# Optimization experiments

Measured on AMD Instinct MI355X. Metric: run time of the kernel, lower is better.

The kernel has to match this reference:

```python
import jax, jax.numpy as jnp
import numpy as np

N_NODES = 100000
IN_DIM = 128
HIDDEN = 256
N_CLASSES = 16
N_EDGES = 1600000
N_GRAPHS = 64


def setup_inputs() -> dict:
    key = jax.random.key(0)
    ks = jax.random.split(key, 12)
    x = jax.random.normal(ks[0], (N_NODES, IN_DIM), dtype=jnp.float32)
    edge_index = jax.random.randint(ks[1], (2, N_EDGES), 0, N_NODES, dtype=jnp.int64)
    batch = jnp.sort(jax.random.randint(ks[2], (N_NODES,), 0, N_GRAPHS, dtype=jnp.int64))
    s = 0.05
    # SAGEConv layer 1: lin_l (on aggregated neighbors, with bias), lin_r (on root, no bias)
    W1l = jax.random.normal(ks[3], (IN_DIM, HIDDEN), dtype=jnp.float32) * s
    b1 = jnp.zeros((HIDDEN,), dtype=jnp.float32)
    W1r = jax.random.normal(ks[4], (IN_DIM, HIDDEN), dtype=jnp.float32) * s
    # SAGEConv layer 2
    W2l = jax.random.normal(ks[5], (HIDDEN, HIDDEN), dtype=jnp.float32) * s
    b2 = jnp.zeros((HIDDEN,), dtype=jnp.float32)
    W2r = jax.random.normal(ks[6], (HIDDEN, HIDDEN), dtype=jnp.float32) * s
    # final classifier
    fcW = jax.random.normal(ks[7], (HIDDEN, N_CLASSES), dtype=jnp.float32) * s
    fcb = jnp.zeros((N_CLASSES,), dtype=jnp.float32)
    return {"x": x, "edge_index": edge_index, "batch": batch,
            "W1l": W1l, "b1": b1, "W1r": W1r,
            "W2l": W2l, "b2": b2, "W2r": W2r,
            "fcW": fcW, "fcb": fcb}


def _sage_conv(x, src, dst, Wl, bl, Wr, n_nodes):
    # mean aggregation of neighbor features onto destination nodes
    agg = jax.ops.segment_sum(x[src], dst, num_segments=n_nodes)      # [N, d]
    deg = jax.ops.segment_sum(jnp.ones(src.shape, x.dtype), dst, num_segments=n_nodes)
    mean = agg / jnp.maximum(deg, 1.0)[:, None]
    # out = lin_l(mean_neighbors) + lin_r(x_root)  (PyG SAGEConv, mean aggr)
    return mean @ Wl + bl + x @ Wr


def reference(x, edge_index, batch, W1l, b1, W1r, W2l, b2, W2r, fcW, fcb):
    src, dst = edge_index[0], edge_index[1]
    h = jax.nn.relu(_sage_conv(x, src, dst, W1l, b1, W1r, N_NODES))
    # dropout is identity in inference mode
    h = jax.nn.relu(_sage_conv(h, src, dst, W2l, b2, W2r, N_NODES))
    # global mean pool over graphs in the batch
    g_sum = jax.ops.segment_sum(h, batch, num_segments=N_GRAPHS)      # [G, d]
    g_cnt = jax.ops.segment_sum(jnp.ones(batch.shape, h.dtype), batch, num_segments=N_GRAPHS)
    g = g_sum / jnp.maximum(g_cnt, 1.0)[:, None]
    return g @ fcW + fcb                                              # [G, num_classes]
```

## Files before the change

kernel.cpp:

```cpp
#include <hip/hip_runtime.h>

#define INDIM 128
#define HID 256
#define NCLS 16
#define NGRAPH 64
#define CHUNK 8192

typedef __bf16 bf16_t;
typedef bf16_t bf16x8 __attribute__((ext_vector_type(8)));
typedef float f32x4 __attribute__((ext_vector_type(4)));

__device__ __forceinline__ float bfu_lo(unsigned v) {
    union { unsigned i; float f; } u; u.i = v << 16; return u.f;
}
__device__ __forceinline__ float bfu_hi(unsigned v) {
    union { unsigned i; float f; } u; u.i = v & 0xffff0000u; return u.f;
}
__device__ __forceinline__ unsigned short f2bf(float f) {
    union { float f; unsigned i; } u; u.f = f;
    unsigned b = u.i;
    return (unsigned short)((b + 0x7fffu + ((b >> 16) & 1u)) >> 16);
}
__device__ __forceinline__ unsigned packbf(float lo, float hi) {
    return (unsigned)f2bf(lo) | ((unsigned)f2bf(hi) << 16);
}

typedef __attribute__((address_space(1))) const unsigned gu32_t;
typedef __attribute__((address_space(3))) unsigned lu32_t;
__device__ __forceinline__ void gl_lds16(const void* g, void* l) {
    __builtin_amdgcn_global_load_lds((gu32_t*)g, (lu32_t*)l, 16, 0, 0);
}

#define IACC(aE, aO, v)                              \
    do {                                             \
        aE[0] += ((v).x & 0x00FF00FFu);              \
        aO[0] += (((v).x >> 8) & 0x00FF00FFu);       \
        aE[1] += ((v).y & 0x00FF00FFu);              \
        aO[1] += (((v).y >> 8) & 0x00FF00FFu);       \
        aE[2] += ((v).z & 0x00FF00FFu);              \
        aO[2] += (((v).z >> 8) & 0x00FF00FFu);       \
        aE[3] += ((v).w & 0x00FF00FFu);              \
        aO[3] += (((v).w >> 8) & 0x00FF00FFu);       \
    } while (0)

__global__ void hist_kernel(const int* __restrict__ dst, int* __restrict__ deg, int E) {
    int e = blockIdx.x * blockDim.x + threadIdx.x;
    if (e < E) atomicAdd(&deg[dst[e]], 1);
}

__global__ void scan1_kernel(const int* __restrict__ deg, int* __restrict__ bsum, int n) {
    __shared__ int s[256];
    int t = threadIdx.x;
    int i = blockIdx.x * 256 + t;
    s[t] = (i < n) ? deg[i] : 0;
    __syncthreads();
    for (int off = 128; off > 0; off >>= 1) {
        if (t < off) s[t] += s[t + off];
        __syncthreads();
    }
    if (t == 0) bsum[blockIdx.x] = s[0];
}

__global__ void scan2_kernel(int* bsum, int nb) {
    __shared__ int s[1024];
    int t = threadIdx.x;
    int v = (t < nb) ? bsum[t] : 0;
    s[t] = v;
    __syncthreads();
    for (int off = 1; off < 1024; off <<= 1) {
        int u = (t >= off) ? s[t - off] : 0;
        __syncthreads();
        s[t] += u;
        __syncthreads();
    }
    if (t < nb) bsum[t] = s[t] - v;
}

__global__ void scan3_kernel(const int* __restrict__ deg, const int* __restrict__ bsum,
                             int* __restrict__ offs, int* __restrict__ gcur, int n) {
    __shared__ int s[256];
    int t = threadIdx.x;
    int i = blockIdx.x * 256 + t;
    int v = (i < n) ? deg[i] : 0;
    s[t] = v;
    __syncthreads();
    for (int off = 1; off < 256; off <<= 1) {
        int u = (t >= off) ? s[t - off] : 0;
        __syncthreads();
        s[t] += u;
        __syncthreads();
    }
    if (i < n) offs[i] = s[t] - v + bsum[blockIdx.x];
    if (t == 0) gcur[blockIdx.x] = bsum[blockIdx.x];
}

__global__ __launch_bounds__(256) void binA_kernel(const int* __restrict__ src,
                                                   const int* __restrict__ dst,
                                                   int* __restrict__ gcur,
                                                   unsigned* __restrict__ tmp,
                                                   int E, int nbuck) {
    __shared__ int hist[512];
    __shared__ int base[512];
    int t = threadIdx.x;
    int e0 = blockIdx.x * CHUNK;
    int e1 = min(e0 + CHUNK, E);
    for (int i = t; i < nbuck; i += 256) hist[i] = 0;
    __syncthreads();
    for (int e = e0 + t; e < e1; e += 256) atomicAdd(&hist[dst[e] >> 8], 1);
    __syncthreads();
    for (int i = t; i < nbuck; i += 256) {
        int c = hist[i];
        base[i] = (c > 0) ? atomicAdd(&gcur[i], c) : 0;
    }
    __syncthreads();
    for (int e = e0 + t; e < e1; e += 256) {
        int d = dst[e];
        int p = atomicAdd(&base[d >> 8], 1);
        tmp[p] = ((unsigned)(d & 255) << 17) | (unsigned)src[e];
    }
}

__global__ __launch_bounds__(256) void binB_kernel(const unsigned* __restrict__ tmp,
                                                   const int* __restrict__ offs,
                                                   int* __restrict__ srclist, int E, int n) {
    __shared__ int cur[256];
    int b = blockIdx.x;
    int node0 = b << 8;
    int nnodes = min(256, n - node0);
    int t = threadIdx.x;
    if (t < nnodes) cur[t] = offs[node0 + t];
    __syncthreads();
    int ebeg = offs[node0];
    int eend = (node0 + 256 < n) ? offs[node0 + 256] : E;
    for (int e = ebeg + t; e < eend; e += 256) {
        unsigned v = tmp[e];
        int p = atomicAdd(&cur[v >> 17], 1);
        srclist[p] = (int)(v & 0x1FFFFu);
    }
}

__global__ void prep_kernel(const float* __restrict__ x, unsigned short* __restrict__ xb,
                            const float* __restrict__ W1l, const float* __restrict__ W1r,
                            unsigned short* __restrict__ Bt1,
                            const float* __restrict__ W2l, const float* __restrict__ W2r,
                            unsigned short* __restrict__ Bt2, float* __restrict__ pmaxx,
                            int castb) {
    __shared__ float wmax[4];
    int b = blockIdx.x, t = threadIdx.x;
    if (b < castb) {
        int i4 = (b * 256 + t) * 4;
        float4 v = *(const float4*)(x + i4);
        *(ushort4*)(xb + i4) = make_ushort4(f2bf(v.x), f2bf(v.y), f2bf(v.z), f2bf(v.w));
        float m = fmaxf(fmaxf(fabsf(v.x), fabsf(v.y)), fmaxf(fabsf(v.z), fabsf(v.w)));
#pragma unroll
        for (int off = 32; off > 0; off >>= 1) m = fmaxf(m, __shfl_xor(m, off));
        if ((t & 63) == 0) wmax[t >> 6] = m;
        __syncthreads();
        if (t == 0)
            pmaxx[b] = fmaxf(fmaxf(wmax[0], wmax[1]), fmaxf(wmax[2], wmax[3]));
    } else if (b < castb + 256) {
        int idx = (b - castb) * 256 + t;
        int nn = idx >> 8, k = idx & 255;
        float v = (k < 128) ? W1l[(size_t)k * 256 + nn] : W1r[(size_t)(k - 128) * 256 + nn];
        Bt1[(size_t)nn * 256 + k] = f2bf(v);
    } else {
        int idx = (b - castb - 256) * 256 + t;
        int nn = idx >> 9, k = idx & 511;
        float v = (k < 256) ? W2l[(size_t)k * 256 + nn] : W2r[(size_t)(k - 256) * 256 + nn];
        Bt2[(size_t)nn * 512 + k] = f2bf(v);
    }
}

__global__ void reducemax_kernel(const float* __restrict__ pmax, int cnt,
                                 float* __restrict__ gmax) {
    __shared__ float wmax[4];
    int t = threadIdx.x;
    float m = 0.f;
    for (int i = t; i < cnt; i += 256) m = fmaxf(m, pmax[i]);
#pragma unroll
    for (int off = 32; off > 0; off >>= 1) m = fmaxf(m, __shfl_xor(m, off));
    if ((t & 63) == 0) wmax[t >> 6] = m;
    __syncthreads();
    if (t == 0) gmax[0] = fmaxf(fmaxf(wmax[0], wmax[1]), fmaxf(wmax[2], wmax[3]));
}

__global__ void quantx_kernel(const float* __restrict__ x, const float* __restrict__ gmaxp,
                              unsigned* __restrict__ xq, int total4) {
    int idx = blockIdx.x * blockDim.x + threadIdx.x;
    if (idx >= total4) return;
    float inv = 127.f / fmaxf(*gmaxp, 1e-20f);
    float4 v = *(const float4*)(x + idx * 4);
    int b0 = (int)fminf(fmaxf(rintf(v.x * inv), -127.f), 127.f) + 128;
    int b1 = (int)fminf(fmaxf(rintf(v.y * inv), -127.f), 127.f) + 128;
    int b2 = (int)fminf(fmaxf(rintf(v.z * inv), -127.f), 127.f) + 128;
    int b3 = (int)fminf(fmaxf(rintf(v.w * inv), -127.f), 127.f) + 128;
    xq[idx] = (unsigned)b0 | ((unsigned)b1 << 8) | ((unsigned)b2 << 16) | ((unsigned)b3 << 24);
}

__global__ void quanth_kernel(const unsigned short* __restrict__ h1, const float* __restrict__ gmaxp,
                              unsigned* __restrict__ hq, int total4) {
    int idx = blockIdx.x * blockDim.x + threadIdx.x;
    if (idx >= total4) return;
    float inv = 127.f / fmaxf(*gmaxp, 1e-20f);
    uint2 v = *(const uint2*)(h1 + idx * 4);
    int b0 = (int)fminf(rintf(bfu_lo(v.x) * inv), 127.f) + 128;
    int b1 = (int)fminf(rintf(bfu_hi(v.x) * inv), 127.f) + 128;
    int b2 = (int)fminf(rintf(bfu_lo(v.y) * inv), 127.f) + 128;
    int b3 = (int)fminf(rintf(bfu_hi(v.y) * inv), 127.f) + 128;
    hq[idx] = (unsigned)b0 | ((unsigned)b1 << 8) | ((unsigned)b2 << 16) | ((unsigned)b3 << 24);
}

__global__ void agg1_kernel(const unsigned char* __restrict__ xq, const int* __restrict__ srclist,
                            const int* __restrict__ offs, const int* __restrict__ deg,
                            const float* __restrict__ gmaxp,
                            unsigned short* __restrict__ mean, int n) {
    int gid = blockIdx.x * blockDim.x + threadIdx.x;
    int node = gid >> 6, lane = gid & 63;
    if (node >= n) return;
    int g = lane >> 3, sub = lane & 7;
    int st = __builtin_amdgcn_readfirstlane(offs[node]);
    int d = __builtin_amdgcn_readfirstlane(deg[node]);
    int end = st + d;
    unsigned aE[4] = {0, 0, 0, 0}, aO[4] = {0, 0, 0, 0};
    unsigned bE[4] = {0, 0, 0, 0}, bO[4] = {0, 0, 0, 0};
    const unsigned char* rb = xq + sub * 16;
    int e = st;
    for (; e + 15 < end; e += 16) {
        int s0 = srclist[e + g];
        int s1 = srclist[e + 8 + g];
        uint4 v0 = *(const uint4*)(rb + (size_t)s0 * 128);
        uint4 v1 = *(const uint4*)(rb + (size_t)s1 * 128);
        IACC(aE, aO, v0);
        IACC(bE, bO, v1);
    }
    for (; e + 7 < end; e += 8) {
        int s0 = srclist[e + g];
        uint4 v0 = *(const uint4*)(rb + (size_t)s0 * 128);
        IACC(aE, aO, v0);
    }
    int rem = end - e;
    if (rem > 0) {
        int s0 = srclist[e + ((g < rem) ? g : 0)];
        uint4 v0 = *(const uint4*)(rb + (size_t)s0 * 128);
        if (g < rem) IACC(aE, aO, v0);
    }
#pragma unroll
    for (int j = 0; j < 4; ++j) {
        unsigned se = aE[j] + bE[j], so = aO[j] + bO[j];
        se += (unsigned)__shfl_xor((int)se, 8);
        se += (unsigned)__shfl_xor((int)se, 16);
        se += (unsigned)__shfl_xor((int)se, 32);
        so += (unsigned)__shfl_xor((int)so, 8);
        so += (unsigned)__shfl_xor((int)so, 16);
        so += (unsigned)__shfl_xor((int)so, 32);
        aE[j] = se;
        aO[j] = so;
    }
    if (g == 0) {
        float sc = (*gmaxp) * (1.f / 127.f);
        float invd = 1.f / fmaxf((float)d, 1.f);
        unsigned o[8];
#pragma unroll
        for (int j = 0; j < 4; ++j) {
            float m0 = sc * (float)((int)(aE[j] & 0xFFFFu) - 128 * d) * invd;
            float m1 = sc * (float)((int)(aO[j] & 0xFFFFu) - 128 * d) * invd;
            float m2 = sc * (float)((int)(aE[j] >> 16) - 128 * d) * invd;
            float m3 = sc * (float)((int)(aO[j] >> 16) - 128 * d) * invd;
            o[j * 2] = packbf(m0, m1);
            o[j * 2 + 1] = packbf(m2, m3);
        }
        uint4* p = (uint4*)(mean + (size_t)node * 128 + sub * 16);
        p[0] = make_uint4(o[0], o[1], o[2], o[3]);
        p[1] = make_uint4(o[4], o[5], o[6], o[7]);
    }
}

__global__ void agg2_kernel(const unsigned char* __restrict__ hq, const int* __restrict__ srclist,
                            const int* __restrict__ offs, const int* __restrict__ deg,
                            const float* __restrict__ gmaxp,
                            unsigned short* __restrict__ mean, int n) {
    int gid = blockIdx.x * blockDim.x + threadIdx.x;
    int node = gid >> 6, lane = gid & 63;
    if (node >= n) return;
    int g = lane >> 4, sub = lane & 15;
    int st = __builtin_amdgcn_readfirstlane(offs[node]);
    int d = __builtin_amdgcn_readfirstlane(deg[node]);
    int end = st + d;
    unsigned aE[4] = {0, 0, 0, 0}, aO[4] = {0, 0, 0, 0};
    unsigned bE[4] = {0, 0, 0, 0}, bO[4] = {0, 0, 0, 0};
    const unsigned char* rb = hq + sub * 16;
    int e = st;
    for (; e + 7 < end; e += 8) {
        int s0 = srclist[e + g];
        int s1 = srclist[e + 4 + g];
        uint4 v0 = *(const uint4*)(rb + (size_t)s0 * 256);
        uint4 v1 = *(const uint4*)(rb + (size_t)s1 * 256);
        IACC(aE, aO, v0);
        IACC(bE, bO, v1);
    }
    for (; e + 3 < end; e += 4) {
        int s0 = srclist[e + g];
        uint4 v0 = *(const uint4*)(rb + (size_t)s0 * 256);
        IACC(aE, aO, v0);
    }
    int rem = end - e;
    if (rem > 0) {
        int s0 = srclist[e + ((g < rem) ? g : 0)];
        uint4 v0 = *(const uint4*)(rb + (size_t)s0 * 256);
        if (g < rem) IACC(aE, aO, v0);
    }
#pragma unroll
    for (int j = 0; j < 4; ++j) {
        unsigned se = aE[j] + bE[j], so = aO[j] + bO[j];
        se += (unsigned)__shfl_xor((int)se, 16);
        se += (unsigned)__shfl_xor((int)se, 32);
        so += (unsigned)__shfl_xor((int)so, 16);
        so += (unsigned)__shfl_xor((int)so, 32);
        aE[j] = se;
        aO[j] = so;
    }
    if (g == 0) {
        float sc = (*gmaxp) * (1.f / 127.f);
        float invd = 1.f / fmaxf((float)d, 1.f);
        unsigned o[8];
#pragma unroll
        for (int j = 0; j < 4; ++j) {
            float m0 = sc * (float)((int)(aE[j] & 0xFFFFu) - 128 * d) * invd;
            float m1 = sc * (float)((int)(aO[j] & 0xFFFFu) - 128 * d) * invd;
            float m2 = sc * (float)((int)(aE[j] >> 16) - 128 * d) * invd;
            float m3 = sc * (float)((int)(aO[j] >> 16) - 128 * d) * invd;
            o[j * 2] = packbf(m0, m1);
            o[j * 2 + 1] = packbf(m2, m3);
        }
        uint4* p = (uint4*)(mean + (size_t)node * 256 + sub * 16);
        p[0] = make_uint4(o[0], o[1], o[2], o[3]);
        p[1] = make_uint4(o[4], o[5], o[6], o[7]);
    }
}

template <int KH>
__global__ __launch_bounds__(256) void gemm_kernel(
        const bf16_t* __restrict__ A1, const bf16_t* __restrict__ A2,
        const bf16_t* __restrict__ Bt, const float* __restrict__ bias,
        unsigned short* __restrict__ H, float* __restrict__ pmax, int M) {
    constexpr int KT = 2 * KH;
    constexpr int NC = KT / 64;
    constexpr int CPH = KH / 64;
    __shared__ unsigned short As[64 * 64];
    __shared__ float wmax[4];
    int t = threadIdx.x, wave = t >> 6, lane = t & 63;
    int quad = lane >> 4, l16 = lane & 15;
    int row0 = blockIdx.x * 64, n0 = wave * 64;

    f32x4 acc[4][4];
#pragma unroll
    for (int i = 0; i < 4; ++i)
#pragma unroll
        for (int j = 0; j < 4; ++j) acc[i][j] = (f32x4)(0.f);

    int rA = wave * 8 + (lane >> 3);
    int kb = lane & 7;
    int kswA = (kb ^ (rA & 7)) << 3;
    unsigned short* ldsA = &As[(size_t)(wave * 8) * 64];
    unsigned short* ldsB = &As[(size_t)(32 + wave * 8) * 64];

    const bf16_t* Bp = Bt + (size_t)(n0 + l16) * KT + quad * 8;

    for (int c = 0; c < NC; ++c) {
        const bf16_t* Ah = (c < CPH) ? A1 : A2;
        int kk = ((c < CPH) ? c : (c - CPH)) * 64;
        gl_lds16(Ah + (size_t)(row0 + rA) * KH + kk + kswA, ldsA);
        gl_lds16(Ah + (size_t)(row0 + 32 + rA) * KH + kk + kswA, ldsB);
        __syncthreads();
        int bk = c * 64;
#pragma unroll
        for (int sub = 0; sub < 2; ++sub) {
            bf16x8 af[4], bfr[4];
#pragma unroll
            for (int mi = 0; mi < 4; ++mi) {
                int r = mi * 16 + l16;
                int qb = sub * 4 + quad;
                af[mi] = *(const bf16x8*)&As[r * 64 + ((qb ^ (r & 7)) << 3)];
            }
#pragma unroll
            for (int ni = 0; ni < 4; ++ni)
                bfr[ni] = *(const bf16x8*)(Bp + (size_t)(ni * 16) * KT + bk + sub * 32);
#pragma unroll
            for (int mi = 0; mi < 4; ++mi)
#pragma unroll
                for (int ni = 0; ni < 4; ++ni)
                    acc[mi][ni] = __builtin_amdgcn_mfma_f32_16x16x32_bf16(
                        af[mi], bfr[ni], acc[mi][ni], 0, 0, 0);
        }
        __syncthreads();
    }

    float bv[4];
#pragma unroll
    for (int ni = 0; ni < 4; ++ni) bv[ni] = bias[n0 + ni * 16 + l16];
    float mloc = 0.f;
#pragma unroll
    for (int mi = 0; mi < 4; ++mi) {
#pragma unroll
        for (int r = 0; r < 4; ++r) {
            int row = row0 + mi * 16 + quad * 4 + r;
            if (row < M) {
#pragma unroll
                for (int ni = 0; ni < 4; ++ni) {
                    int col = n0 + ni * 16 + l16;
                    float hv = fmaxf(acc[mi][ni][r] + bv[ni], 0.f);
                    mloc = fmaxf(mloc, hv);
                    H[(size_t)row * 256 + col] = f2bf(hv);
                }
            }
        }
    }
    if (pmax) {
#pragma unroll
        for (int off = 32; off > 0; off >>= 1) mloc = fmaxf(mloc, __shfl_xor(mloc, off));
        if (lane == 0) wmax[wave] = mloc;
        __syncthreads();
        if (t == 0)
            pmax[blockIdx.x] = fmaxf(fmaxf(wmax[0], wmax[1]), fmaxf(wmax[2], wmax[3]));
    }
}

__global__ __launch_bounds__(256) void pool_kernel(const unsigned short* __restrict__ h2,
                                                   const int* __restrict__ batch,
                                                   float* __restrict__ g, float* __restrict__ cnt,
                                                   int n) {
    int col = threadIdx.x;
    int row0 = blockIdx.x * 64;
    int rend = min(row0 + 64, n);
    float acc = 0.f;
    int cur = -1, seglen = 0;
    int r = row0;
    for (; r + 3 < rend; r += 4) {
        int b0 = batch[r], b1 = batch[r + 1], b2 = batch[r + 2], b3 = batch[r + 3];
        unsigned short v0 = h2[(size_t)r * 256 + col];
        unsigned short v1 = h2[(size_t)(r + 1) * 256 + col];
        unsigned short v2 = h2[(size_t)(r + 2) * 256 + col];
        unsigned short v3 = h2[(size_t)(r + 3) * 256 + col];
        int bs[4] = {b0, b1, b2, b3};
        unsigned short vs[4] = {v0, v1, v2, v3};
#pragma unroll
        for (int j = 0; j < 4; ++j) {
            if (bs[j] != cur) {
                if (cur >= 0) {
                    atomicAdd(&g[cur * 256 + col], acc);
                    if (col == 0) atomicAdd(&cnt[cur], (float)seglen);
                }
                acc = 0.f; cur = bs[j]; seglen = 0;
            }
            union { unsigned i; float f; } u;
            u.i = ((unsigned)vs[j]) << 16;
            acc += u.f;
            seglen++;
        }
    }
    for (; r < rend; ++r) {
        int b = batch[r];
        if (b != cur) {
            if (cur >= 0) {
                atomicAdd(&g[cur * 256 + col], acc);
                if (col == 0) atomicAdd(&cnt[cur], (float)seglen);
            }
            acc = 0.f; cur = b; seglen = 0;
        }
        union { unsigned i; float f; } u;
        u.i = ((unsigned)h2[(size_t)r * 256 + col]) << 16;
        acc += u.f;
        seglen++;
    }
    if (cur >= 0) {
        atomicAdd(&g[cur * 256 + col], acc);
        if (col == 0) atomicAdd(&cnt[cur], (float)seglen);
    }
}

__global__ void final_kernel(const float* __restrict__ g, const float* __restrict__ cnt,
                             const float* __restrict__ fcW, const float* __restrict__ fcb,
                             float* __restrict__ out) {
    int t = threadIdx.x;
    for (int o = t; o < NGRAPH * NCLS; o += 256) {
        int gi = o >> 4, c = o & 15;
        float inv = 1.f / fmaxf(cnt[gi], 1.f);
        float dot = 0.f;
        for (int k = 0; k < 256; ++k) dot += g[gi * 256 + k] * fcW[k * 16 + c];
        out[o] = dot * inv + fcb[c];
    }
}

extern "C" void kernel_launch(void* const* d_in, const int* in_sizes, int n_in, void* d_out,
                              int out_size, void* d_ws, size_t ws_size, hipStream_t stream) {
    const float* x   = (const float*)d_in[0];
    const int* edge  = (const int*)d_in[1];
    const int* batch = (const int*)d_in[2];
    const float* W1l = (const float*)d_in[3];
    const float* b1  = (const float*)d_in[4];
    const float* W1r = (const float*)d_in[5];
    const float* W2l = (const float*)d_in[6];
    const float* b2  = (const float*)d_in[7];
    const float* W2r = (const float*)d_in[8];
    const float* fcW = (const float*)d_in[9];
    const float* fcb = (const float*)d_in[10];
    float* out = (float*)d_out;

    const int n = in_sizes[0] / INDIM;
    const int E = in_sizes[1] / 2;
    const int* src = edge;
    const int* dst = edge + E;
    const int nbuck = (n + 255) >> 8;

    char* ws = (char*)d_ws;
    size_t off = 0;
    auto alloc = [&](size_t bytes) {
        size_t p = off;
        off = (off + bytes + 511) & ~(size_t)511;
        return p;
    };
    size_t offs_o    = alloc((size_t)n * 4);
    size_t deg_o     = alloc((size_t)n * 4);
    size_t cnt_o     = alloc(64 * 4);
    size_t g_o       = alloc(64 * 256 * 4);
    size_t gmax_o    = alloc(8);
    size_t zero_end  = off;
    size_t pmax_o    = alloc(12544 * 4);
    size_t bsum_o    = alloc(1024 * 4);
    size_t gcur_o    = alloc(512 * 4);
    size_t srclist_o = alloc((size_t)E * 4);
    size_t bt1_o     = alloc(256 * 256 * 2);
    size_t bt2_o     = alloc(256 * 512 * 2);
    size_t xbm2_o    = alloc((size_t)n * 256 * 2);
    size_t mean1_o   = alloc((size_t)n * 128 * 2);
    size_t h1_o      = alloc((size_t)n * 256 * 2);
    size_t h2_o      = alloc((size_t)n * 256 * 2);

    int*   offs    = (int*)(ws + offs_o);
    int*   deg     = (int*)(ws + deg_o);
    float* cnt     = (float*)(ws + cnt_o);
    float* g       = (float*)(ws + g_o);
    float* gmaxx   = (float*)(ws + gmax_o);
    float* gmaxh   = (float*)(ws + gmax_o + 4);
    float* pmax    = (float*)(ws + pmax_o);
    int*   bsum    = (int*)(ws + bsum_o);
    int*   gcur    = (int*)(ws + gcur_o);
    int*   srclist = (int*)(ws + srclist_o);
    unsigned short* Bt1   = (unsigned short*)(ws + bt1_o);
    unsigned short* Bt2   = (unsigned short*)(ws + bt2_o);
    unsigned short* xb16  = (unsigned short*)(ws + xbm2_o);
    unsigned char*  xq8   = (unsigned char*)(ws + xbm2_o + (size_t)n * 256);
    unsigned short* mean2 = (unsigned short*)(ws + xbm2_o);
    unsigned short* mean1 = (unsigned short*)(ws + mean1_o);
    unsigned short* h1b   = (unsigned short*)(ws + h1_o);
    unsigned*       tmp   = (unsigned*)(ws + h2_o);
    unsigned char*  hq8   = (unsigned char*)(ws + h2_o + (size_t)n * 256);
    unsigned short* h2b   = (unsigned short*)(ws + h2_o);

    hipMemsetAsync(ws + deg_o, 0, zero_end - deg_o, stream);

    int eb = (E + 255) / 256;
    int nb = (n + 255) / 256;
    hist_kernel<<<eb, 256, 0, stream>>>(dst, deg, E);
    scan1_kernel<<<nb, 256, 0, stream>>>(deg, bsum, n);
    scan2_kernel<<<1, 1024, 0, stream>>>(bsum, nb);
    scan3_kernel<<<nb, 256, 0, stream>>>(deg, bsum, offs, gcur, n);
    binA_kernel<<<(E + CHUNK - 1) / CHUNK, 256, 0, stream>>>(src, dst, gcur, tmp, E, nbuck);
    binB_kernel<<<nbuck, 256, 0, stream>>>(tmp, offs, srclist, E, n);

    int castb = n * INDIM / 4 / 256;
    prep_kernel<<<castb + 256 + 512, 256, 0, stream>>>(x, xb16, W1l, W1r, Bt1, W2l, W2r, Bt2,
                                                       pmax, castb);
    reducemax_kernel<<<1, 256, 0, stream>>>(pmax, castb, gmaxx);
    int xq4 = n * INDIM / 4;
    quantx_kernel<<<(xq4 + 255) / 256, 256, 0, stream>>>(x, gmaxx, (unsigned*)xq8, xq4);

    int aggb = (n * 64 + 255) / 256;
    int gemmb = (n + 63) / 64;

    agg1_kernel<<<aggb, 256, 0, stream>>>(xq8, srclist, offs, deg, gmaxx, mean1, n);
    gemm_kernel<128><<<gemmb, 256, 0, stream>>>(
        (const bf16_t*)mean1, (const bf16_t*)xb16, (const bf16_t*)Bt1, b1, h1b, pmax, n);
    reducemax_kernel<<<1, 256, 0, stream>>>(pmax, gemmb, gmaxh);
    int hq4 = n * HID / 4;
    quanth_kernel<<<(hq4 + 255) / 256, 256, 0, stream>>>(h1b, gmaxh, (unsigned*)hq8, hq4);
    agg2_kernel<<<aggb, 256, 0, stream>>>(hq8, srclist, offs, deg, gmaxh, mean2, n);
    gemm_kernel<256><<<gemmb, 256, 0, stream>>>(
        (const bf16_t*)mean2, (const bf16_t*)h1b, (const bf16_t*)Bt2, b2, h2b,
        (float*)nullptr, n);

    pool_kernel<<<(n + 63) / 64, 256, 0, stream>>>(h2b, batch, g, cnt, n);
    final_kernel<<<1, 256, 0, stream>>>(g, cnt, fcW, fcb, out);
}
```

Measured before the change: 554.7 us.

## Fuse layer-2 GEMM epilogue with global mean pooling, drop h2 materialization

The second SAGE GEMM now applies bias and ReLU in registers and sums rows directly into per-graph accumulators with atomics, so the bf16 h2 buffer is never written and the separate pool kernel no longer has to read it back. Graph node counts move to a small shared-memory histogram kernel. This removes one full N×256 write and read and a launch. In exchange, pooling happens in fp32 from accumulators rather than bf16-rounded values, and the GEMM epilogue gains a loop over the graphs each row block spans.

```diff
diff --git a/kernel.cpp b/kernel.cpp
--- a/kernel.cpp
+++ b/kernel.cpp
@@ -182,6 +182,17 @@
     if ((t & 63) == 0) wmax[t >> 6] = m;
     __syncthreads();
     if (t == 0) gmax[0] = fmaxf(fmaxf(wmax[0], wmax[1]), fmaxf(wmax[2], wmax[3]));
+}
+
+__global__ void cnt_kernel(const int* __restrict__ batch, float* __restrict__ cnt, int n) {
+    __shared__ int h[64];
+    int t = threadIdx.x;
+    if (t < 64) h[t] = 0;
+    __syncthreads();
+    int i = blockIdx.x * 256 + t;
+    if (i < n) atomicAdd(&h[batch[i]], 1);
+    __syncthreads();
+    if (t < 64 && h[t] > 0) atomicAdd(&cnt[t], (float)h[t]);
 }
 
 __global__ void quantx_kernel(const float* __restrict__ x, const float* __restrict__ gmaxp,
@@ -425,56 +436,92 @@
     }
 }
 
-__global__ __launch_bounds__(256) void pool_kernel(const unsigned short* __restrict__ h2,
-                                                   const int* __restrict__ batch,
-                                                   float* __restrict__ g, float* __restrict__ cnt,
-                                                   int n) {
-    int col = threadIdx.x;
-    int row0 = blockIdx.x * 64;
-    int rend = min(row0 + 64, n);
-    float acc = 0.f;
-    int cur = -1, seglen = 0;
-    int r = row0;
-    for (; r + 3 < rend; r += 4) {
-        int b0 = batch[r], b1 = batch[r + 1], b2 = batch[r + 2], b3 = batch[r + 3];
-        unsigned short v0 = h2[(size_t)r * 256 + col];
-        unsigned short v1 = h2[(size_t)(r + 1) * 256 + col];
-        unsigned short v2 = h2[(size_t)(r + 2) * 256 + col];
-        unsigned short v3 = h2[(size_t)(r + 3) * 256 + col];
-        int bs[4] = {b0, b1, b2, b3};
-        unsigned short vs[4] = {v0, v1, v2, v3};
-#pragma unroll
-        for (int j = 0; j < 4; ++j) {
-            if (bs[j] != cur) {
-                if (cur >= 0) {
-                    atomicAdd(&g[cur * 256 + col], acc);
-                    if (col == 0) atomicAdd(&cnt[cur], (float)seglen);
+__global__ __launch_bounds__(256) void gemm2p_kernel(
+        const bf16_t* __restrict__ A1, const bf16_t* __restrict__ A2,
+        const bf16_t* __restrict__ Bt, const float* __restrict__ bias,
+        const int* __restrict__ batch, float* __restrict__ g, int M) {
+    constexpr int KH = 256, KT = 512, NC = 8, CPH = 4;
+    __shared__ unsigned short As[64 * 64];
+    __shared__ int sbatch[64];
+    int t = threadIdx.x, wave = t >> 6, lane = t & 63;
+    int quad = lane >> 4, l16 = lane & 15;
+    int row0 = blockIdx.x * 64, n0 = wave * 64;
+
+    if (t < 64) sbatch[t] = (row0 + t < M) ? batch[row0 + t] : -1;
+
+    f32x4 acc[4][4];
+#pragma unroll
+    for (int i = 0; i < 4; ++i)
+#pragma unroll
+        for (int j = 0; j < 4; ++j) acc[i][j] = (f32x4)(0.f);
+
+    int rA = wave * 8 + (lane >> 3);
+    int kb = lane & 7;
+    int kswA = (kb ^ (rA & 7)) << 3;
+    unsigned short* ldsA = &As[(size_t)(wave * 8) * 64];
+    unsigned short* ldsB = &As[(size_t)(32 + wave * 8) * 64];
+
+    const bf16_t* Bp = Bt + (size_t)(n0 + l16) * KT + quad * 8;
+
+    for (int c = 0; c < NC; ++c) {
+        const bf16_t* Ah = (c < CPH) ? A1 : A2;
+        int kk = ((c < CPH) ? c : (c - CPH)) * 64;
+        gl_lds16(Ah + (size_t)(row0 + rA) * KH + kk + kswA, ldsA);
+        gl_lds16(Ah + (size_t)(row0 + 32 + rA) * KH + kk + kswA, ldsB);
+        __syncthreads();
+        int bk = c * 64;
+#pragma unroll
+        for (int sub = 0; sub < 2; ++sub) {
+            bf16x8 af[4], bfr[4];
+#pragma unroll
+            for (int mi = 0; mi < 4; ++mi) {
+                int r = mi * 16 + l16;
+                int qb = sub * 4 + quad;
+                af[mi] = *(const bf16x8*)&As[r * 64 + ((qb ^ (r & 7)) << 3)];
+            }
+#pragma unroll
+            for (int ni = 0; ni < 4; ++ni)
+                bfr[ni] = *(const bf16x8*)(Bp + (size_t)(ni * 16) * KT + bk + sub * 32);
+#pragma unroll
+            for (int mi = 0; mi < 4; ++mi)
+#pragma unroll
+                for (int ni = 0; ni < 4; ++ni)
+                    acc[mi][ni] = __builtin_amdgcn_mfma_f32_16x16x32_bf16(
+                        af[mi], bfr[ni], acc[mi][ni], 0, 0, 0);
+        }
+        __syncthreads();
+    }
+
+    float bv[4];
+#pragma unroll
+    for (int ni = 0; ni < 4; ++ni) bv[ni] = bias[n0 + ni * 16 + l16];
+
+    int rlast = min(63, M - 1 - row0);
+    int b0 = sbatch[0], b1 = sbatch[rlast];
+    for (int gb = b0; gb <= b1; ++gb) {
+        float colsum[4] = {0.f, 0.f, 0.f, 0.f};
+#pragma unroll
+        for (int mi = 0; mi < 4; ++mi) {
+#pragma unroll
+            for (int r = 0; r < 4; ++r) {
+                int rl = mi * 16 + quad * 4 + r;
+                if (sbatch[rl] == gb) {
+#pragma unroll
+                    for (int ni = 0; ni < 4; ++ni)
+                        colsum[ni] += fmaxf(acc[mi][ni][r] + bv[ni], 0.f);
                 }
-                acc = 0.f; cur = bs[j]; seglen = 0;
             }
-            union { unsigned i; float f; } u;
-            u.i = ((unsigned)vs[j]) << 16;
-            acc += u.f;
-            seglen++;
-        }
-    }
-    for (; r < rend; ++r) {
-        int b = batch[r];
-        if (b != cur) {
-            if (cur >= 0) {
-                atomicAdd(&g[cur * 256 + col], acc);
-                if (col == 0) atomicAdd(&cnt[cur], (float)seglen);
-            }
-            acc = 0.f; cur = b; seglen = 0;
-        }
-        union { unsigned i; float f; } u;
-        u.i = ((unsigned)h2[(size_t)r * 256 + col]) << 16;
-        acc += u.f;
-        seglen++;
-    }
-    if (cur >= 0) {
-        atomicAdd(&g[cur * 256 + col], acc);
-        if (col == 0) atomicAdd(&cnt[cur], (float)seglen);
+        }
+#pragma unroll
+        for (int ni = 0; ni < 4; ++ni) {
+            colsum[ni] += __shfl_xor(colsum[ni], 16);
+            colsum[ni] += __shfl_xor(colsum[ni], 32);
+        }
+        if (lane < 16) {
+#pragma unroll
+            for (int ni = 0; ni < 4; ++ni)
+                atomicAdd(&g[gb * 256 + n0 + ni * 16 + l16], colsum[ni]);
+        }
     }
 }
 
@@ -534,7 +581,7 @@
     size_t xbm2_o    = alloc((size_t)n * 256 * 2);
     size_t mean1_o   = alloc((size_t)n * 128 * 2);
     size_t h1_o      = alloc((size_t)n * 256 * 2);
-    size_t h2_o      = alloc((size_t)n * 256 * 2);
+    size_t aux_o     = alloc((size_t)n * 256 * 2);
 
     int*   offs    = (int*)(ws + offs_o);
     int*   deg     = (int*)(ws + deg_o);
@@ -553,9 +600,8 @@
     unsigned short* mean2 = (unsigned short*)(ws + xbm2_o);
     unsigned short* mean1 = (unsigned short*)(ws + mean1_o);
     unsigned short* h1b   = (unsigned short*)(ws + h1_o);
-    unsigned*       tmp   = (unsigned*)(ws + h2_o);
-    unsigned char*  hq8   = (unsigned char*)(ws + h2_o + (size_t)n * 256);
-    unsigned short* h2b   = (unsigned short*)(ws + h2_o);
+    unsigned*       tmp   = (unsigned*)(ws + aux_o);
+    unsigned char*  hq8   = (unsigned char*)(ws + aux_o + (size_t)n * 256);
 
     hipMemsetAsync(ws + deg_o, 0, zero_end - deg_o, stream);
 
@@ -572,6 +618,7 @@
     prep_kernel<<<castb + 256 + 512, 256, 0, stream>>>(x, xb16, W1l, W1r, Bt1, W2l, W2r, Bt2,
                                                        pmax, castb);
     reducemax_kernel<<<1, 256, 0, stream>>>(pmax, castb, gmaxx);
+    cnt_kernel<<<nb, 256, 0, stream>>>(batch, cnt, n);
     int xq4 = n * INDIM / 4;
     quantx_kernel<<<(xq4 + 255) / 256, 256, 0, stream>>>(x, gmaxx, (unsigned*)xq8, xq4);
 
@@ -585,10 +632,8 @@
     int hq4 = n * HID / 4;
     quanth_kernel<<<(hq4 + 255) / 256, 256, 0, stream>>>(h1b, gmaxh, (unsigned*)hq8, hq4);
     agg2_kernel<<<aggb, 256, 0, stream>>>(hq8, srclist, offs, deg, gmaxh, mean2, n);
-    gemm_kernel<256><<<gemmb, 256, 0, stream>>>(
-        (const bf16_t*)mean2, (const bf16_t*)h1b, (const bf16_t*)Bt2, b2, h2b,
-        (float*)nullptr, n);
-
-    pool_kernel<<<(n + 63) / 64, 256, 0, stream>>>(h2b, batch, g, cnt, n);
+    gemm2p_kernel<<<gemmb, 256, 0, stream>>>(
+        (const bf16_t*)mean2, (const bf16_t*)h1b, (const bf16_t*)Bt2, b2, batch, g, n);
+
     final_kernel<<<1, 256, 0, stream>>>(g, cnt, fcW, fcb, out);
 }
```

Result: faster. 536.4 us (-3.3%).
